# Optimization experiments

Measured on AMD Instinct MI355X. Metric: run time of the kernel, lower is better.

Reference implementation:

```python
import jax, jax.numpy as jnp
import numpy as np

B, T, C = 32, 1024, 256   # T must equal block_size for the mask broadcast to be valid
HS = 64                   # head_size


def setup_inputs() -> dict:
    key = jax.random.key(0)
    kx, kk, kq, kv = jax.random.split(key, 4)
    s = 1.0 / np.sqrt(C)  # nn.Linear default-ish scale
    return {
        "x": jax.random.normal(kx, (B, T, C), dtype=jnp.float32),
        "Wk": jax.random.uniform(kk, (HS, C), dtype=jnp.float32, minval=-s, maxval=s),
        "Wq": jax.random.uniform(kq, (HS, C), dtype=jnp.float32, minval=-s, maxval=s),
        "Wv": jax.random.uniform(kv, (HS, C), dtype=jnp.float32, minval=-s, maxval=s),
    }


def reference(x, Wk, Wq, Wv):
    # projections: nn.Linear(bias=False) -> x @ W^T
    k = jnp.einsum('btc,hc->bth', x, Wk)  # [B,T,HS]
    q = jnp.einsum('btc,hc->bth', x, Wq)
    v = jnp.einsum('btc,hc->bth', x, Wv)
    # fresh cache + T == block_size  =>  k_cache = k, v_cache = v
    wei = jnp.einsum('bth,bsh->bts', q, k) / np.sqrt(HS)  # [B,T,T]
    causal = jnp.tril(jnp.ones((T, T), dtype=bool))
    wei = jnp.where(causal, wei, -jnp.inf)
    wei = jax.nn.softmax(wei, axis=-1)  # dropout p=0 -> identity
    out = jnp.einsum('bts,bsh->bth', wei, v)  # [B,T,HS]
    return out
```

## Files before the change

kernel.cpp:

```cpp
#include <hip/hip_runtime.h>
#include <hip/hip_bf16.h>
#include <math.h>


#define B_  32
#define T_  1024
#define C_  256
#define HS_ 64
#define QSCALE 0.1803368801111204f

typedef __attribute__((ext_vector_type(8))) short bf16x8;
typedef __attribute__((ext_vector_type(4))) float f32x4;

static __device__ __forceinline__ unsigned short f2bf(float f) {
    unsigned u = __builtin_bit_cast(unsigned, f);
    u += 0x7FFFu + ((u >> 16) & 1u);
    return (unsigned short)(u >> 16);
}

static __device__ __forceinline__ float fexp2(float x) {
#if __has_builtin(__builtin_amdgcn_exp2f)
    return __builtin_amdgcn_exp2f(x);
#else
    return exp2f(x);
#endif
}

__global__ __launch_bounds__(256) void proj_kernel(
    const float* __restrict__ x, const float* __restrict__ Wk,
    const float* __restrict__ Wq, const float* __restrict__ Wv,
    unsigned short* __restrict__ fqk, unsigned short* __restrict__ vt)
{
    __shared__ unsigned short xs[64][40];
    __shared__ unsigned short ws[192][40];
    const int tid = threadIdx.x;
    const int lane = tid & 63, w = tid >> 6;
    const int q4 = lane >> 4, l15 = lane & 15;
    const int m0 = blockIdx.x * 64;

    f32x4 acc[3][4];
    #pragma unroll
    for (int a = 0; a < 3; ++a)
        #pragma unroll
        for (int b = 0; b < 4; ++b) acc[a][b] = (f32x4)0.0f;

    for (int c0 = 0; c0 < C_; c0 += 32) {
        __syncthreads();
        #pragma unroll
        for (int it = 0; it < 2; ++it) {
            int qq = tid + it * 256;
            int row = qq >> 3, col = (qq & 7) << 2;
            float4 v = *(const float4*)&x[(size_t)(m0 + row) * C_ + c0 + col];
            unsigned lo = f2bf(v.x) | ((unsigned)f2bf(v.y) << 16);
            unsigned hi = f2bf(v.z) | ((unsigned)f2bf(v.w) << 16);
            *(uint2*)&xs[row][col] = make_uint2(lo, hi);
        }
        #pragma unroll
        for (int it = 0; it < 6; ++it) {
            int qq = tid + it * 256;
            int row = qq >> 3, col = (qq & 7) << 2;
            const float* src = (row < 64) ? &Wk[(size_t)row * C_]
                             : (row < 128) ? &Wq[(size_t)(row - 64) * C_]
                             : &Wv[(size_t)(row - 128) * C_];
            float sc = (row >= 64 && row < 128) ? QSCALE : 1.0f;
            float4 v = *(const float4*)&src[c0 + col];
            unsigned lo = f2bf(v.x * sc) | ((unsigned)f2bf(v.y * sc) << 16);
            unsigned hi = f2bf(v.z * sc) | ((unsigned)f2bf(v.w * sc) << 16);
            *(uint2*)&ws[row][col] = make_uint2(lo, hi);
        }
        __syncthreads();
        bf16x8 a[3], b[4];
        #pragma unroll
        for (int nt = 0; nt < 3; ++nt) a[nt] = *(const bf16x8*)&ws[48 * w + nt * 16 + l15][q4 * 8];
        #pragma unroll
        for (int mt = 0; mt < 4; ++mt) b[mt] = *(const bf16x8*)&xs[mt * 16 + l15][q4 * 8];
        #pragma unroll
        for (int nt = 0; nt < 3; ++nt)
            #pragma unroll
            for (int mt = 0; mt < 4; ++mt)
                acc[nt][mt] = __builtin_amdgcn_mfma_f32_16x16x32_bf16(a[nt], b[mt], acc[nt][mt], 0, 0, 0);
    }

    #pragma unroll
    for (int nt = 0; nt < 3; ++nt) {
        const int nb = 48 * w + nt * 16 + q4 * 4;
        #pragma unroll
        for (int mt = 0; mt < 4; ++mt) {
            const int m = m0 + mt * 16 + l15;
            f32x4 v = acc[nt][mt];
            if (nb < 128) {
                unsigned lo = f2bf(v.x) | ((unsigned)f2bf(v.y) << 16);
                unsigned hi = f2bf(v.z) | ((unsigned)f2bf(v.w) << 16);
                *(uint2*)&fqk[(size_t)m * 128 + nb] = make_uint2(lo, hi);
            } else {
                const int batch = m >> 10, s = m & 1023;
                #pragma unroll
                for (int r = 0; r < 4; ++r) {
                    float vv = (r == 0) ? v.x : (r == 1) ? v.y : (r == 2) ? v.z : v.w;
                    vt[((size_t)batch * 64 + (nb - 128 + r)) * 1024 + s] = f2bf(vv);
                }
            }
        }
    }
}

__global__ __launch_bounds__(64) void attn_kernel(
    const unsigned short* __restrict__ fqk,
    const unsigned short* __restrict__ vt,
    float* __restrict__ out)
{
    const int lane = threadIdx.x;
    const int q4 = lane >> 4, l15 = lane & 15;
    const int batch = blockIdx.x & 31;
    const int qt = 31 - (blockIdx.x >> 5);
    const int q0 = qt * 32;
    const int ns = (qt >> 1) + 1;

    __shared__ unsigned short Ps[32][72];

    bf16x8 qf[2][2];
    #pragma unroll
    for (int it = 0; it < 2; ++it)
        #pragma unroll
        for (int kc = 0; kc < 2; ++kc)
            qf[it][kc] = *(const bf16x8*)&fqk[(size_t)(batch * T_ + q0 + it * 16 + l15) * 128 + 64 + kc * 32 + q4 * 8];

    f32x4 o[4][2];
    #pragma unroll
    for (int ht = 0; ht < 4; ++ht)
        #pragma unroll
        for (int it = 0; it < 2; ++it) o[ht][it] = (f32x4)0.0f;
    float l[2] = {0.f, 0.f};

    const unsigned short* kbase = &fqk[(size_t)(batch * T_) * 128];
    const unsigned short* vbase = &vt[(size_t)batch * 64 * 1024];

    bf16x8 ak[4][2];
    #pragma unroll
    for (int st16 = 0; st16 < 4; ++st16)
        #pragma unroll
        for (int kc = 0; kc < 2; ++kc)
            ak[st16][kc] = *(const bf16x8*)&kbase[(size_t)(st16 * 16 + l15) * 128 + kc * 32 + q4 * 8];

    for (int st = 0; st < ns; ++st) {
        const int s0 = st * 64;
        f32x4 s[4][2];
        #pragma unroll
        for (int st16 = 0; st16 < 4; ++st16)
            #pragma unroll
            for (int it = 0; it < 2; ++it) {
                f32x4 c = (f32x4)0.0f;
                c = __builtin_amdgcn_mfma_f32_16x16x32_bf16(ak[st16][0], qf[it][0], c, 0, 0, 0);
                c = __builtin_amdgcn_mfma_f32_16x16x32_bf16(ak[st16][1], qf[it][1], c, 0, 0, 0);
                s[st16][it] = c;
            }
        bf16x8 av[4][2];
        #pragma unroll
        for (int ht = 0; ht < 4; ++ht)
            #pragma unroll
            for (int kc = 0; kc < 2; ++kc)
                av[ht][kc] = *(const bf16x8*)&vbase[(size_t)(ht * 16 + l15) * 1024 + s0 + kc * 32 + q4 * 8];
        if (st + 1 < ns) {
            #pragma unroll
            for (int st16 = 0; st16 < 4; ++st16)
                #pragma unroll
                for (int kc = 0; kc < 2; ++kc)
                    ak[st16][kc] = *(const bf16x8*)&kbase[(size_t)(s0 + 64 + st16 * 16 + l15) * 128 + kc * 32 + q4 * 8];
        }
        const bool last = (st == ns - 1);
        #pragma unroll
        for (int st16 = 0; st16 < 4; ++st16) {
            #pragma unroll
            for (int it = 0; it < 2; ++it) {
                const int iloc = it * 16 + l15;
                float p[4];
                #pragma unroll
                for (int r = 0; r < 4; ++r) {
                    float pv = fexp2(s[st16][it][r]);
                    if (last) {
                        int sl = st16 * 16 + q4 * 4 + r;
                        if (s0 + sl > q0 + iloc) pv = 0.0f;
                    }
                    p[r] = pv;
                    l[it] += pv;
                }
                unsigned lo = f2bf(p[0]) | ((unsigned)f2bf(p[1]) << 16);
                unsigned hi = f2bf(p[2]) | ((unsigned)f2bf(p[3]) << 16);
                *(uint2*)&Ps[iloc][st16 * 16 + q4 * 4] = make_uint2(lo, hi);
            }
        }
        #pragma unroll
        for (int it = 0; it < 2; ++it) {
            bf16x8 bp0 = *(const bf16x8*)&Ps[it * 16 + l15][q4 * 8];
            bf16x8 bp1 = *(const bf16x8*)&Ps[it * 16 + l15][32 + q4 * 8];
            #pragma unroll
            for (int ht = 0; ht < 4; ++ht) {
                o[ht][it] = __builtin_amdgcn_mfma_f32_16x16x32_bf16(av[ht][0], bp0, o[ht][it], 0, 0, 0);
                o[ht][it] = __builtin_amdgcn_mfma_f32_16x16x32_bf16(av[ht][1], bp1, o[ht][it], 0, 0, 0);
            }
        }
    }

    #pragma unroll
    for (int it = 0; it < 2; ++it) {
        float lf = l[it];
        lf += __shfl_xor(lf, 16);
        lf += __shfl_xor(lf, 32);
        l[it] = 1.0f / lf;
    }
    #pragma unroll
    for (int ht = 0; ht < 4; ++ht)
        #pragma unroll
        for (int it = 0; it < 2; ++it) {
            f32x4 v = o[ht][it];
            float4 res = make_float4(v.x * l[it], v.y * l[it], v.z * l[it], v.w * l[it]);
            *(float4*)&out[(size_t)(batch * T_ + q0 + it * 16 + l15) * HS_ + ht * 16 + q4 * 4] = res;
        }
}

extern "C" void kernel_launch(void* const* d_in, const int* in_sizes, int n_in,
                              void* d_out, int out_size, void* d_ws, size_t ws_size,
                              hipStream_t stream) {
    (void)in_sizes; (void)n_in; (void)out_size; (void)ws_size;
    const float* x  = (const float*)d_in[0];
    const float* Wk = (const float*)d_in[1];
    const float* Wq = (const float*)d_in[2];
    const float* Wv = (const float*)d_in[3];

    unsigned short* fqk = (unsigned short*)d_ws;
    unsigned short* vtb = (unsigned short*)((char*)d_ws + (size_t)32768 * 128 * 2);

    hipLaunchKernelGGL(proj_kernel, dim3(512), dim3(256), 0, stream,
                       x, Wk, Wq, Wv, fqk, vtb);
    hipLaunchKernelGGL(attn_kernel, dim3(1024), dim3(64), 0, stream,
                       fqk, vtb, (float*)d_out);
}
```

Measured before the change: 123.4 us.

## Split attention KV loop across four waves, pre-convert weights, drop LDS in projection

The attention kernel now runs 256 threads per block. Each of four waves handles every fourth 64-key tile, and the partial outputs and row sums are combined through shared memory at the end, which parallelises the long serial KV loop of each query tile. A separate prep kernel converts the weights to bf16 once, so the projection kernel can load x and the weights straight into registers without LDS staging or barriers. Float-to-bf16 packing now uses a byte-perm with round-half-up instead of round-to-nearest-even. The cost is an extra launch, the cross-wave reduction, and the loss of the previous K prefetch.

After: 121.6 us. Within noise of the previous version (-1.5%).

```diff
diff --git a/kernel.cpp b/kernel.cpp
--- a/kernel.cpp
+++ b/kernel.cpp
@@ -17,7 +17,11 @@
     u += 0x7FFFu + ((u >> 16) & 1u);
     return (unsigned short)(u >> 16);
 }
-
+static __device__ __forceinline__ unsigned pack_bf2(float a, float b) {
+    unsigned ua = __builtin_bit_cast(unsigned, a) + 0x8000u;
+    unsigned ub = __builtin_bit_cast(unsigned, b) + 0x8000u;
+    return __builtin_amdgcn_perm(ub, ua, 0x07060302u);
+}
 static __device__ __forceinline__ float fexp2(float x) {
 #if __has_builtin(__builtin_amdgcn_exp2f)
     return __builtin_amdgcn_exp2f(x);
@@ -26,97 +30,95 @@
 #endif
 }
 
+__global__ __launch_bounds__(256) void prep_kernel(
+    const float* __restrict__ Wk, const float* __restrict__ Wq,
+    const float* __restrict__ Wv, unsigned short* __restrict__ wbf)
+{
+    const int idx = blockIdx.x * 256 + threadIdx.x;
+    const int row = idx >> 6, c4 = (idx & 63) << 2;
+    const float* src; float sc = 1.0f;
+    if (row < 64)       src = &Wk[(size_t)row * C_];
+    else if (row < 128) { src = &Wq[(size_t)(row - 64) * C_]; sc = QSCALE; }
+    else                src = &Wv[(size_t)(row - 128) * C_];
+    float4 v = *(const float4*)&src[c4];
+    uint2 o = make_uint2(pack_bf2(v.x * sc, v.y * sc), pack_bf2(v.z * sc, v.w * sc));
+    *(uint2*)&wbf[(size_t)row * C_ + c4] = o;
+}
+
 __global__ __launch_bounds__(256) void proj_kernel(
-    const float* __restrict__ x, const float* __restrict__ Wk,
-    const float* __restrict__ Wq, const float* __restrict__ Wv,
+    const float* __restrict__ x, const unsigned short* __restrict__ wbf,
     unsigned short* __restrict__ fqk, unsigned short* __restrict__ vt)
 {
-    __shared__ unsigned short xs[64][40];
-    __shared__ unsigned short ws[192][40];
     const int tid = threadIdx.x;
     const int lane = tid & 63, w = tid >> 6;
+    const int wm = w & 1, wn = w >> 1;
     const int q4 = lane >> 4, l15 = lane & 15;
-    const int m0 = blockIdx.x * 64;
-
-    f32x4 acc[3][4];
-    #pragma unroll
-    for (int a = 0; a < 3; ++a)
-        #pragma unroll
-        for (int b = 0; b < 4; ++b) acc[a][b] = (f32x4)0.0f;
+    const int mbase = blockIdx.x * 64 + wm * 32;
+
+    f32x4 acc[6][2];
+    #pragma unroll
+    for (int nt = 0; nt < 6; ++nt)
+        #pragma unroll
+        for (int mt = 0; mt < 2; ++mt) acc[nt][mt] = (f32x4)0.0f;
 
     for (int c0 = 0; c0 < C_; c0 += 32) {
-        __syncthreads();
-        #pragma unroll
-        for (int it = 0; it < 2; ++it) {
-            int qq = tid + it * 256;
-            int row = qq >> 3, col = (qq & 7) << 2;
-            float4 v = *(const float4*)&x[(size_t)(m0 + row) * C_ + c0 + col];
-            unsigned lo = f2bf(v.x) | ((unsigned)f2bf(v.y) << 16);
-            unsigned hi = f2bf(v.z) | ((unsigned)f2bf(v.w) << 16);
-            *(uint2*)&xs[row][col] = make_uint2(lo, hi);
-        }
-        #pragma unroll
-        for (int it = 0; it < 6; ++it) {
-            int qq = tid + it * 256;
-            int row = qq >> 3, col = (qq & 7) << 2;
-            const float* src = (row < 64) ? &Wk[(size_t)row * C_]
-                             : (row < 128) ? &Wq[(size_t)(row - 64) * C_]
-                             : &Wv[(size_t)(row - 128) * C_];
-            float sc = (row >= 64 && row < 128) ? QSCALE : 1.0f;
-            float4 v = *(const float4*)&src[c0 + col];
-            unsigned lo = f2bf(v.x * sc) | ((unsigned)f2bf(v.y * sc) << 16);
-            unsigned hi = f2bf(v.z * sc) | ((unsigned)f2bf(v.w * sc) << 16);
-            *(uint2*)&ws[row][col] = make_uint2(lo, hi);
-        }
-        __syncthreads();
-        bf16x8 a[3], b[4];
-        #pragma unroll
-        for (int nt = 0; nt < 3; ++nt) a[nt] = *(const bf16x8*)&ws[48 * w + nt * 16 + l15][q4 * 8];
-        #pragma unroll
-        for (int mt = 0; mt < 4; ++mt) b[mt] = *(const bf16x8*)&xs[mt * 16 + l15][q4 * 8];
-        #pragma unroll
-        for (int nt = 0; nt < 3; ++nt)
-            #pragma unroll
-            for (int mt = 0; mt < 4; ++mt)
-                acc[nt][mt] = __builtin_amdgcn_mfma_f32_16x16x32_bf16(a[nt], b[mt], acc[nt][mt], 0, 0, 0);
-    }
-
-    #pragma unroll
-    for (int nt = 0; nt < 3; ++nt) {
-        const int nb = 48 * w + nt * 16 + q4 * 4;
-        #pragma unroll
-        for (int mt = 0; mt < 4; ++mt) {
-            const int m = m0 + mt * 16 + l15;
+        bf16x8 bx[2];
+        #pragma unroll
+        for (int mt = 0; mt < 2; ++mt) {
+            const float* px = &x[(size_t)(mbase + mt * 16 + l15) * C_ + c0 + q4 * 8];
+            float4 v0 = *(const float4*)px;
+            float4 v1 = *(const float4*)(px + 4);
+            union { bf16x8 v; unsigned u[4]; } t;
+            t.u[0] = pack_bf2(v0.x, v0.y); t.u[1] = pack_bf2(v0.z, v0.w);
+            t.u[2] = pack_bf2(v1.x, v1.y); t.u[3] = pack_bf2(v1.z, v1.w);
+            bx[mt] = t.v;
+        }
+        #pragma unroll
+        for (int nt = 0; nt < 6; ++nt) {
+            bf16x8 a = *(const bf16x8*)&wbf[(size_t)(wn * 96 + nt * 16 + l15) * C_ + c0 + q4 * 8];
+            #pragma unroll
+            for (int mt = 0; mt < 2; ++mt)
+                acc[nt][mt] = __builtin_amdgcn_mfma_f32_16x16x32_bf16(a, bx[mt], acc[nt][mt], 0, 0, 0);
+        }
+    }
+
+    #pragma unroll
+    for (int nt = 0; nt < 6; ++nt) {
+        const int nbase = wn * 96 + nt * 16 + q4 * 4;
+        #pragma unroll
+        for (int mt = 0; mt < 2; ++mt) {
+            const int m = mbase + mt * 16 + l15;
             f32x4 v = acc[nt][mt];
-            if (nb < 128) {
-                unsigned lo = f2bf(v.x) | ((unsigned)f2bf(v.y) << 16);
-                unsigned hi = f2bf(v.z) | ((unsigned)f2bf(v.w) << 16);
-                *(uint2*)&fqk[(size_t)m * 128 + nb] = make_uint2(lo, hi);
+            if (nbase < 128) {
+                uint2 o = make_uint2(pack_bf2(v.x, v.y), pack_bf2(v.z, v.w));
+                *(uint2*)&fqk[(size_t)m * 128 + nbase] = o;
             } else {
-                const int batch = m >> 10, s = m & 1023;
-                #pragma unroll
-                for (int r = 0; r < 4; ++r) {
-                    float vv = (r == 0) ? v.x : (r == 1) ? v.y : (r == 2) ? v.z : v.w;
-                    vt[((size_t)batch * 64 + (nb - 128 + r)) * 1024 + s] = f2bf(vv);
-                }
+                const int batch = m >> 10, s = m & 1023, h = nbase - 128;
+                vt[((size_t)batch * 64 + h + 0) * 1024 + s] = f2bf(v.x);
+                vt[((size_t)batch * 64 + h + 1) * 1024 + s] = f2bf(v.y);
+                vt[((size_t)batch * 64 + h + 2) * 1024 + s] = f2bf(v.z);
+                vt[((size_t)batch * 64 + h + 3) * 1024 + s] = f2bf(v.w);
             }
         }
     }
 }
 
-__global__ __launch_bounds__(64) void attn_kernel(
+__global__ __launch_bounds__(256) void attn_kernel(
     const unsigned short* __restrict__ fqk,
     const unsigned short* __restrict__ vt,
     float* __restrict__ out)
 {
-    const int lane = threadIdx.x;
+    __shared__ __align__(16) char smem[34816];
+
+    const int tid = threadIdx.x;
+    const int lane = tid & 63, w = tid >> 6;
     const int q4 = lane >> 4, l15 = lane & 15;
     const int batch = blockIdx.x & 31;
     const int qt = 31 - (blockIdx.x >> 5);
     const int q0 = qt * 32;
     const int ns = (qt >> 1) + 1;
 
-    __shared__ unsigned short Ps[32][72];
+    unsigned short (*Ps)[72] = (unsigned short(*)[72])(smem + w * 4608);
 
     bf16x8 qf[2][2];
     #pragma unroll
@@ -135,87 +137,95 @@
     const unsigned short* kbase = &fqk[(size_t)(batch * T_) * 128];
     const unsigned short* vbase = &vt[(size_t)batch * 64 * 1024];
 
-    bf16x8 ak[4][2];
-    #pragma unroll
-    for (int st16 = 0; st16 < 4; ++st16)
-        #pragma unroll
-        for (int kc = 0; kc < 2; ++kc)
-            ak[st16][kc] = *(const bf16x8*)&kbase[(size_t)(st16 * 16 + l15) * 128 + kc * 32 + q4 * 8];
-
-    for (int st = 0; st < ns; ++st) {
+    for (int st = w; st < ns; st += 4) {
         const int s0 = st * 64;
-        f32x4 s[4][2];
-        #pragma unroll
-        for (int st16 = 0; st16 < 4; ++st16)
+        const bool last = (st == ns - 1);
+        #pragma unroll
+        for (int hf = 0; hf < 2; ++hf) {
+            const int sh = s0 + hf * 32;
+            bf16x8 ak[2][2];
+            #pragma unroll
+            for (int st16 = 0; st16 < 2; ++st16)
+                #pragma unroll
+                for (int kc = 0; kc < 2; ++kc)
+                    ak[st16][kc] = *(const bf16x8*)&kbase[(size_t)(sh + st16 * 16 + l15) * 128 + kc * 32 + q4 * 8];
+            bf16x8 av[4];
+            #pragma unroll
+            for (int ht = 0; ht < 4; ++ht)
+                av[ht] = *(const bf16x8*)&vbase[(size_t)(ht * 16 + l15) * 1024 + sh + q4 * 8];
+            f32x4 s[2][2];
+            #pragma unroll
+            for (int st16 = 0; st16 < 2; ++st16)
+                #pragma unroll
+                for (int it = 0; it < 2; ++it) {
+                    f32x4 c = (f32x4)0.0f;
+                    c = __builtin_amdgcn_mfma_f32_16x16x32_bf16(ak[st16][0], qf[it][0], c, 0, 0, 0);
+                    c = __builtin_amdgcn_mfma_f32_16x16x32_bf16(ak[st16][1], qf[it][1], c, 0, 0, 0);
+                    s[st16][it] = c;
+                }
+            #pragma unroll
+            for (int st16 = 0; st16 < 2; ++st16)
+                #pragma unroll
+                for (int it = 0; it < 2; ++it) {
+                    const int iloc = it * 16 + l15;
+                    float p[4];
+                    #pragma unroll
+                    for (int r = 0; r < 4; ++r) {
+                        float pv = fexp2(s[st16][it][r]);
+                        if (last) {
+                            int sl = sh + st16 * 16 + q4 * 4 + r;
+                            if (sl > q0 + iloc) pv = 0.0f;
+                        }
+                        p[r] = pv;
+                        l[it] += pv;
+                    }
+                    uint2 pw = make_uint2(pack_bf2(p[0], p[1]), pack_bf2(p[2], p[3]));
+                    *(uint2*)&Ps[iloc][hf * 32 + st16 * 16 + q4 * 4] = pw;
+                }
             #pragma unroll
             for (int it = 0; it < 2; ++it) {
-                f32x4 c = (f32x4)0.0f;
-                c = __builtin_amdgcn_mfma_f32_16x16x32_bf16(ak[st16][0], qf[it][0], c, 0, 0, 0);
-                c = __builtin_amdgcn_mfma_f32_16x16x32_bf16(ak[st16][1], qf[it][1], c, 0, 0, 0);
-                s[st16][it] = c;
+                bf16x8 bp = *(const bf16x8*)&Ps[it * 16 + l15][hf * 32 + q4 * 8];
+                #pragma unroll
+                for (int ht = 0; ht < 4; ++ht)
+                    o[ht][it] = __builtin_amdgcn_mfma_f32_16x16x32_bf16(av[ht], bp, o[ht][it], 0, 0, 0);
             }
-        bf16x8 av[4][2];
-        #pragma unroll
-        for (int ht = 0; ht < 4; ++ht)
-            #pragma unroll
-            for (int kc = 0; kc < 2; ++kc)
-                av[ht][kc] = *(const bf16x8*)&vbase[(size_t)(ht * 16 + l15) * 1024 + s0 + kc * 32 + q4 * 8];
-        if (st + 1 < ns) {
-            #pragma unroll
-            for (int st16 = 0; st16 < 4; ++st16)
-                #pragma unroll
-                for (int kc = 0; kc < 2; ++kc)
-                    ak[st16][kc] = *(const bf16x8*)&kbase[(size_t)(s0 + 64 + st16 * 16 + l15) * 128 + kc * 32 + q4 * 8];
-        }
-        const bool last = (st == ns - 1);
-        #pragma unroll
-        for (int st16 = 0; st16 < 4; ++st16) {
-            #pragma unroll
-            for (int it = 0; it < 2; ++it) {
-                const int iloc = it * 16 + l15;
-                float p[4];
-                #pragma unroll
-                for (int r = 0; r < 4; ++r) {
-                    float pv = fexp2(s[st16][it][r]);
-                    if (last) {
-                        int sl = st16 * 16 + q4 * 4 + r;
-                        if (s0 + sl > q0 + iloc) pv = 0.0f;
-                    }
-                    p[r] = pv;
-                    l[it] += pv;
-                }
-                unsigned lo = f2bf(p[0]) | ((unsigned)f2bf(p[1]) << 16);
-                unsigned hi = f2bf(p[2]) | ((unsigned)f2bf(p[3]) << 16);
-                *(uint2*)&Ps[iloc][st16 * 16 + q4 * 4] = make_uint2(lo, hi);
-            }
-        }
-        #pragma unroll
-        for (int it = 0; it < 2; ++it) {
-            bf16x8 bp0 = *(const bf16x8*)&Ps[it * 16 + l15][q4 * 8];
-            bf16x8 bp1 = *(const bf16x8*)&Ps[it * 16 + l15][32 + q4 * 8];
-            #pragma unroll
-            for (int ht = 0; ht < 4; ++ht) {
-                o[ht][it] = __builtin_amdgcn_mfma_f32_16x16x32_bf16(av[ht][0], bp0, o[ht][it], 0, 0, 0);
-                o[ht][it] = __builtin_amdgcn_mfma_f32_16x16x32_bf16(av[ht][1], bp1, o[ht][it], 0, 0, 0);
-            }
         }
     }
 
     #pragma unroll
     for (int it = 0; it < 2; ++it) {
-        float lf = l[it];
-        lf += __shfl_xor(lf, 16);
-        lf += __shfl_xor(lf, 32);
-        l[it] = 1.0f / lf;
-    }
+        l[it] += __shfl_xor(l[it], 16);
+        l[it] += __shfl_xor(l[it], 32);
+    }
+
+    __syncthreads();
+    float4* ocomb = (float4*)smem;
+    float*  lcomb = (float*)(smem + 32768);
     #pragma unroll
     for (int ht = 0; ht < 4; ++ht)
         #pragma unroll
         for (int it = 0; it < 2; ++it) {
             f32x4 v = o[ht][it];
-            float4 res = make_float4(v.x * l[it], v.y * l[it], v.z * l[it], v.w * l[it]);
-            *(float4*)&out[(size_t)(batch * T_ + q0 + it * 16 + l15) * HS_ + ht * 16 + q4 * 4] = res;
-        }
+            ocomb[((w * 4 + ht) * 2 + it) * 64 + lane] = make_float4(v.x, v.y, v.z, v.w);
+        }
+    #pragma unroll
+    for (int it = 0; it < 2; ++it) lcomb[(w * 2 + it) * 64 + lane] = l[it];
+    __syncthreads();
+
+    #pragma unroll
+    for (int it = 0; it < 2; ++it) {
+        float4 a = make_float4(0.f, 0.f, 0.f, 0.f);
+        float lt = 0.f;
+        #pragma unroll
+        for (int src = 0; src < 4; ++src) {
+            float4 t = ocomb[((src * 4 + w) * 2 + it) * 64 + lane];
+            a.x += t.x; a.y += t.y; a.z += t.z; a.w += t.w;
+            lt += lcomb[(src * 2 + it) * 64 + lane];
+        }
+        float inv = 1.0f / lt;
+        float4 res = make_float4(a.x * inv, a.y * inv, a.z * inv, a.w * inv);
+        *(float4*)&out[(size_t)(batch * T_ + q0 + it * 16 + l15) * HS_ + w * 16 + q4 * 4] = res;
+    }
 }
 
 extern "C" void kernel_launch(void* const* d_in, const int* in_sizes, int n_in,
@@ -227,11 +237,11 @@
     const float* Wq = (const float*)d_in[2];
     const float* Wv = (const float*)d_in[3];
 
-    unsigned short* fqk = (unsigned short*)d_ws;
-    unsigned short* vtb = (unsigned short*)((char*)d_ws + (size_t)32768 * 128 * 2);
-
-    hipLaunchKernelGGL(proj_kernel, dim3(512), dim3(256), 0, stream,
-                       x, Wk, Wq, Wv, fqk, vtb);
-    hipLaunchKernelGGL(attn_kernel, dim3(1024), dim3(64), 0, stream,
-                       fqk, vtb, (float*)d_out);
-}
+    unsigned short* wbf = (unsigned short*)d_ws;
+    unsigned short* fqk = (unsigned short*)((char*)d_ws + 98304);
+    unsigned short* vtb = (unsigned short*)((char*)d_ws + 98304 + (size_t)32768 * 128 * 2);
+
+    hipLaunchKernelGGL(prep_kernel, dim3(48),   dim3(256), 0, stream, Wk, Wq, Wv, wbf);
+    hipLaunchKernelGGL(proj_kernel, dim3(512),  dim3(256), 0, stream, x, wbf, fqk, vtb);
+    hipLaunchKernelGGL(attn_kernel, dim3(1024), dim3(256), 0, stream, fqk, vtb, (float*)d_out);
+}
```
